# Kernel optimization log

Hardware: AMD Instinct MI355X
Metric: run time of the kernel (lower is better)

## Reference

```python
import jax, jax.numpy as jnp
import numpy as np

N = 20000      # nodes
E = 160000     # edges
F_IN = 64      # node_feature_dim
HID = 256      # hidden_dim (= per-head out_channels, concat=False)
HEADS = 4
OUT = 2
BN_EPS = 1e-5


def setup_inputs() -> dict:
    key = jax.random.key(0)
    ks = jax.random.split(key, 24)
    s = 0.02

    def w(k, shape):
        return jax.random.normal(k, shape, jnp.float32) * s

    return {
        "node_feature": jax.random.normal(ks[0], (N, F_IN), jnp.float32),
        "edge_index": jax.random.randint(ks[1], (2, E), 0, N, jnp.int32),
        # layer 1 (in=F_IN)
        "wq1": w(ks[2], (F_IN, HEADS * HID)), "bq1": w(ks[3], (HEADS * HID,)),
        "wk1": w(ks[4], (F_IN, HEADS * HID)), "bk1": w(ks[5], (HEADS * HID,)),
        "wv1": w(ks[6], (F_IN, HEADS * HID)), "bv1": w(ks[7], (HEADS * HID,)),
        "ws1": w(ks[8], (F_IN, HID)),        "bs1": w(ks[9], (HID,)),
        # layer 2 (in=HID)
        "wq2": w(ks[10], (HID, HEADS * HID)), "bq2": w(ks[11], (HEADS * HID,)),
        "wk2": w(ks[12], (HID, HEADS * HID)), "bk2": w(ks[13], (HEADS * HID,)),
        "wv2": w(ks[14], (HID, HEADS * HID)), "bv2": w(ks[15], (HEADS * HID,)),
        "ws2": w(ks[16], (HID, HID)),         "bs2": w(ks[17], (HID,)),
        # batch norm affine
        "bn_gamma": jnp.ones((HID,), jnp.float32) + w(ks[18], (HID,)),
        "bn_beta": w(ks[19], (HID,)),
        # final linear
        "lin_w": w(ks[20], (HID, OUT)), "lin_b": w(ks[21], (OUT,)),
    }


def _transformer_conv(x, src, dst, wq, bq, wk, bk, wv, bv, ws, bs):
    """PyG TransformerConv, heads=HEADS, concat=False (mean over heads), root_weight."""
    n = x.shape[0]
    q = (x @ wq + bq).reshape(n, HEADS, HID)   # [N,H,C]
    k = (x @ wk + bk).reshape(n, HEADS, HID)
    v = (x @ wv + bv).reshape(n, HEADS, HID)
    # per-edge attention logits: q_i . k_j / sqrt(C)   (message j->i, i = dst)
    alpha = jnp.einsum('ehc,ehc->eh', q[dst], k[src]) / jnp.sqrt(jnp.float32(HID))  # [E,H]
    # scatter-softmax over incoming edges of each target node
    m = jax.ops.segment_max(alpha, dst, num_segments=n)
    m = jnp.where(jnp.isfinite(m), m, 0.0)  # nodes with no in-edges
    ex = jnp.exp(alpha - m[dst])
    denom = jax.ops.segment_sum(ex, dst, num_segments=n)
    a = ex / (denom[dst] + 1e-16)                          # [E,H]
    out = jax.ops.segment_sum(v[src] * a[..., None], dst, num_segments=n)  # [N,H,C]
    return out.mean(axis=1) + x @ ws + bs                  # concat=False -> head mean; + skip


def reference(node_feature, edge_index,
              wq1, bq1, wk1, bk1, wv1, bv1, ws1, bs1,
              wq2, bq2, wk2, bk2, wv2, bv2, ws2, bs2,
              bn_gamma, bn_beta, lin_w, lin_b):
    src, dst = edge_index[0], edge_index[1]
    x = _transformer_conv(node_feature, src, dst, wq1, bq1, wk1, bk1, wv1, bv1, ws1, bs1)
    x = _transformer_conv(x, src, dst, wq2, bq2, wk2, bk2, wv2, bv2, ws2, bs2)
    # BatchNorm1d (training mode: batch statistics, biased variance)
    mu = x.mean(axis=0)
    var = jnp.mean(jnp.square(x - mu), axis=0)
    x = bn_gamma * (x - mu) / jnp.sqrt(var + BN_EPS) + bn_beta
    rsu_embedding = x[0:1]                     # [1, HID]
    logits = jax.nn.relu(x @ lin_w + lin_b)    # [N, OUT]
    action_prob = jax.nn.softmax(logits, axis=1)
    return (action_prob, rsu_embedding)
```

## Files before the change

### kernel.cpp

```cpp
#include <hip/hip_runtime.h>
#include <hip/hip_bf16.h>
#include <math.h>

#define DI __device__ __forceinline__

constexpr int NN   = 20000;
constexpr int NE   = 160000;
constexpr int FIN  = 64;
constexpr int HIDC = 256;

typedef __attribute__((ext_vector_type(8))) short short8;
typedef __attribute__((ext_vector_type(4))) float f32x4;

DI float bf2f(unsigned short u) { return __uint_as_float(((unsigned)u) << 16); }

DI void gld16(const void* g, void* l) {
  __builtin_amdgcn_global_load_lds((const __attribute__((address_space(1))) unsigned*)g,
                                   (__attribute__((address_space(3))) unsigned*)l, 16, 0, 0);
}

__global__ void k_prep(const float* __restrict__ x, __hip_bfloat16* __restrict__ xb,
                       const int* __restrict__ dst, int* __restrict__ deg) {
  int gid = blockIdx.x * 256 + threadIdx.x;
  if (gid < NN * FIN) xb[gid] = __float2bfloat16(x[gid]);
  if (gid < NE) atomicAdd(&deg[dst[gid]], 1);
}

__global__ void k_scan(const int* __restrict__ deg, int* __restrict__ offs,
                       int* __restrict__ cursor, int n_) {
  __shared__ int part[1024];
  int tid = threadIdx.x;
  const int CH = (n_ + 1023) >> 10;
  int base = tid * CH;
  int s = 0;
  for (int i = 0; i < CH; ++i) { int idx = base + i; if (idx < n_) s += deg[idx]; }
  part[tid] = s;
  __syncthreads();
  for (int off = 1; off < 1024; off <<= 1) {
    int v = (tid >= off) ? part[tid - off] : 0;
    __syncthreads();
    part[tid] += v;
    __syncthreads();
  }
  int run = (tid == 0) ? 0 : part[tid - 1];
  for (int i = 0; i < CH; ++i) {
    int idx = base + i;
    if (idx < n_) { offs[idx] = run; cursor[idx] = run; run += deg[idx]; }
  }
  if (tid == 1023) offs[n_] = run;
}

__global__ void k_scatter(const int* __restrict__ dst, int* __restrict__ cursor,
                          int* __restrict__ eid, int e_) {
  int e = blockIdx.x * blockDim.x + threadIdx.x;
  if (e < e_) {
    int p = atomicAdd(&cursor[dst[e]], 1);
    eid[p] = e;
  }
}

__global__ void k_sortsse(const int* __restrict__ offs, int* __restrict__ eid,
                          const int* __restrict__ src, int* __restrict__ sse, int n_) {
  int n = blockIdx.x * 256 + threadIdx.x;
  if (n >= n_) return;
  int s0 = offs[n], s1 = offs[n + 1];
  for (int i = s0 + 1; i < s1; ++i) {
    int v = eid[i];
    int j = i - 1;
    while (j >= s0 && eid[j] > v) { eid[j + 1] = eid[j]; --j; }
    eid[j + 1] = v;
  }
  for (int i = s0; i < s1; ++i) sse[i] = src[eid[i]];
}

__global__ void k_tr(const float* __restrict__ wq, const float* __restrict__ wk,
                     float* __restrict__ WqT, float* __restrict__ WkT, int IN_) {
  int gid = blockIdx.x * 256 + threadIdx.x;
  if (gid >= 1024 * IN_) return;
  int k = gid % IN_, j = gid / IN_;
  WqT[gid] = wq[(size_t)k * 1024 + j];
  WkT[gid] = wk[(size_t)k * 1024 + j];
}

template <int IN>
__global__ void k_mfill(const float* __restrict__ WqT, const float* __restrict__ WkT,
                        const float* __restrict__ bq, const float* __restrict__ bk,
                        const float* __restrict__ ws, const float* __restrict__ bs,
                        __hip_bfloat16* __restrict__ Wt, float* __restrict__ biasp) {
  constexpr int YW = 4 * IN;
  constexpr int CPB = 256 / IN;
  int k = threadIdx.x % IN;
  int sub = threadIdx.x / IN;
  int c = blockIdx.x * CPB + sub;
  float val = 0.f, bval = 0.f;
  if (c < YW) {
    int h = c / IN, i = c % IN;
    const float* wqp = WqT + (size_t)(h * 256) * IN + k;
    const float* wkp = WkT + (size_t)(h * 256) * IN + i;
    float s = 0.f;
#pragma unroll 4
    for (int j = 0; j < 256; ++j) s = fmaf(wqp[(size_t)j * IN], wkp[(size_t)j * IN], s);
    val = s;
  } else if (c < YW + 256) {
    int sc = c - YW;
    val = ws[(size_t)k * 256 + sc];
    bval = bs[sc];
  } else if (c < YW + 260) {
    int h = c - (YW + 256);
    const float* wqp = WqT + (size_t)(h * 256) * IN + k;
    const float* bkp = bk + h * 256;
    float s = 0.f;
#pragma unroll 4
    for (int j = 0; j < 256; ++j) s = fmaf(wqp[(size_t)j * IN], bkp[j], s);
    val = s;
    if (k == 0) {
      float bb = 0.f;
      for (int j = 0; j < 256; ++j) bb = fmaf(bq[h * 256 + j], bk[h * 256 + j], bb);
      bval = bb;
    }
  } else if (c < YW + 264) {
    int h = c - (YW + 260);
    const float* wkp = WkT + (size_t)(h * 256) * IN + k;
    const float* bqp = bq + h * 256;
    float s = 0.f;
#pragma unroll 4
    for (int j = 0; j < 256; ++j) s = fmaf(wkp[(size_t)j * IN], bqp[j], s);
    val = s;
  }
  Wt[(size_t)c * IN + k] = __float2bfloat16(val);
  if (k == 0) biasp[c] = bval;
}

template <int IN>
__global__ void k_pack2(const float* __restrict__ wv, const float* __restrict__ bv,
                        __hip_bfloat16* __restrict__ Wt2, float* __restrict__ bias2) {
  constexpr int K2 = 4 * IN;
  int gid = blockIdx.x * 256 + threadIdx.x;
  int col = gid / K2, k = gid % K2;
  int h = k / IN, d = k % IN;
  Wt2[gid] = __float2bfloat16(0.25f * wv[(size_t)d * 1024 + h * 256 + col]);
  if (k == 0)
    bias2[col] = 0.25f * (bv[col] + bv[256 + col] + bv[512 + col] + bv[768 + col]);
}

template <int IN>
__global__ __launch_bounds__(64, 2) void k_gemm1(
    const __hip_bfloat16* __restrict__ X, const __hip_bfloat16* __restrict__ Wt,
    const float* __restrict__ biasp,
    __hip_bfloat16* __restrict__ Ybuf, float* __restrict__ skipf,
    float* __restrict__ CDbuf, int nrows, int NCB, int NCH, int TPC, int RT) {
  __shared__ char lds[16384 + 2304];
  const int l = threadIdx.x;
  constexpr int K = IN;
  constexpr int YW = 4 * IN;
  const int nwg = NCB * NCH;
  const int per = nwg >> 3;
  const int w = (blockIdx.x & 7) * per + (blockIdx.x >> 3);
  const int chunk = w / NCB;
  const int ct = w % NCB;
  const int bn = ct * 64;
  const int t0 = chunk * TPC;
  int t1 = t0 + TPC; if (t1 > RT) t1 = RT;
  constexpr int KT = K / 64;
  constexpr int NS = K / 32;

  const int lm = l & 15, lk = l >> 4;

  short8 bfr[4 * NS];
  {
    const __hip_bfloat16* bp = Wt + (size_t)(bn + lm) * K + lk * 8;
#pragma unroll
    for (int n = 0; n < 4; ++n)
#pragma unroll
      for (int s = 0; s < NS; ++s)
        bfr[n * NS + s] = *(const short8*)(bp + (size_t)n * 16 * K + s * 32);
  }
  float bia[4];
#pragma unroll
  for (int n = 0; n < 4; ++n) bia[n] = biasp[bn + n * 16 + lm];

  const int mode = (bn < YW) ? 0 : ((bn < YW + 256) ? 1 : 2);

  const int jrow = l >> 3;
  const int cslot = (l & 7) ^ jrow;
  auto STAGE = [&](int buf, int t, int kt) {
    char* db = lds + buf * 8192;
#pragma unroll
    for (int j = 0; j < 8; ++j) {
      int r = t * 64 + j * 8 + jrow;
      if (r >= nrows) r = nrows - 1;
      gld16(X + (size_t)r * K + kt * 64 + cslot * 8, db + j * 1024 + l * 16);
    }
  };

  int buf = 0;
  STAGE(0, t0, 0);
  for (int t = t0; t < t1; ++t) {
    f32x4 acc[4][4] = {};
#pragma unroll
    for (int kt = 0; kt < KT; ++kt) {
      int nt = t, nk = kt + 1;
      if (nk == KT) { nt = (t + 1 < t1) ? t + 1 : t; nk = 0; }
      STAGE(buf ^ 1, nt, nk);
      asm volatile("s_waitcnt vmcnt(8)" ::: "memory");
      const char* db = lds + buf * 8192;
#pragma unroll
      for (int s2 = 0; s2 < 2; ++s2) {
        short8 a[4];
#pragma unroll
        for (int m = 0; m < 4; ++m) {
          int row = m * 16 + lm;
          a[m] = *(const short8*)(db + row * 128 + (((s2 * 4 + lk) ^ (lm & 7)) * 16));
        }
#pragma unroll
        for (int m = 0; m < 4; ++m)
#pragma unroll
          for (int n = 0; n < 4; ++n)
            acc[m][n] = __builtin_amdgcn_mfma_f32_16x16x32_bf16(
                a[m], bfr[n * NS + kt * 2 + s2], acc[m][n], 0, 0, 0);
      }
      buf ^= 1;
    }

    const int tbase = t * 64;
    if (mode == 0) {
      char* sc = lds + 16384;
      const int srow = l >> 2, qc = l & 3;
#pragma unroll
      for (int m = 0; m < 4; ++m) {
#pragma unroll
        for (int n = 0; n < 4; ++n)
#pragma unroll
          for (int r = 0; r < 4; ++r)
            *(__hip_bfloat16*)(sc + (lk * 4 + r) * 144 + (n * 16 + lm) * 2) =
                __float2bfloat16(acc[m][n][r] + bia[n]);
        const char* sr = sc + srow * 144 + qc * 32;
        short8 ta = *(const short8*)(sr);
        short8 tb = *(const short8*)(sr + 16);
        int grow = tbase + m * 16 + srow;
        if (grow < nrows) {
          ushort* o = (ushort*)Ybuf + (size_t)grow * YW + bn + qc * 16;
          *(short8*)o = ta;
          *(short8*)(o + 8) = tb;
        }
      }
    } else if (mode == 1) {
      const int cb = bn - YW;
#pragma unroll
      for (int m = 0; m < 4; ++m)
#pragma unroll
        for (int n = 0; n < 4; ++n)
#pragma unroll
          for (int r = 0; r < 4; ++r) {
            int row = tbase + m * 16 + lk * 4 + r;
            if (row < nrows) skipf[(size_t)row * HIDC + cb + n * 16 + lm] = acc[m][n][r] + bia[n];
          }
    } else {
#pragma unroll
      for (int m = 0; m < 4; ++m)
#pragma unroll
        for (int n = 0; n < 4; ++n) {
          int cl = n * 16 + lm;
          if (cl < 8) {
#pragma unroll
            for (int r = 0; r < 4; ++r) {
              int row = tbase + m * 16 + lk * 4 + r;
              if (row < nrows) CDbuf[(size_t)row * 8 + cl] = acc[m][n][r] + bia[n];
            }
          }
        }
    }
  }
  asm volatile("s_waitcnt vmcnt(0)" ::: "memory");
}

template <int IN, bool F32OUT>
__global__ __launch_bounds__(512) void k_attn_out(
    const __hip_bfloat16* __restrict__ Ybuf, const __hip_bfloat16* __restrict__ Xs,
    const float* __restrict__ CD, const int* __restrict__ offs,
    const int* __restrict__ sse, const __hip_bfloat16* __restrict__ Wt2,
    const float* __restrict__ bias2, const float* __restrict__ skipf,
    void* __restrict__ outp) {
  constexpr int K2 = 4 * IN;
  constexpr int DPL = IN / 16;
  constexpr int YW = 4 * IN;
  __shared__ __align__(16) char Zs[32 * K2 * 2];
  const int w = threadIdx.x >> 6, lane = threadIdx.x & 63;
  const int h4 = lane >> 4, j = lane & 15;
  const int nbase = blockIdx.x * 32;

  for (int u = 0; u < 4; ++u) {
    const int zrow = w * 4 + u;
    const int n = nbase + zrow;
    char* zp = Zs + zrow * (K2 * 2);
    const int sw = (zrow & 7) << 4;
    const int s0 = offs[n];
    const int deg = offs[n + 1] - s0;
    const int cb = (h4 * IN + j * DPL) * 2;

    if (deg == 0) {
      if constexpr (IN == 256) {
        short8 z8 = {};
        *(short8*)(zp + (cb ^ sw)) = z8;
        *(short8*)(zp + ((cb + 16) ^ sw)) = z8;
      } else {
        short4 z4 = {(short)0, (short)0, (short)0, (short)0};
        *(short4*)(zp + (cb ^ sw)) = z4;
      }
      continue;
    }

    float y[DPL];
    {
      const ushort* yr = (const ushort*)Ybuf + (size_t)n * YW + h4 * IN + j * DPL;
      if constexpr (IN == 256) {
        short8 y0 = *(const short8*)yr;
        short8 y1 = *(const short8*)(yr + 8);
#pragma unroll
        for (int d = 0; d < 8; ++d) {
          y[d] = bf2f((unsigned short)y0[d]);
          y[8 + d] = bf2f((unsigned short)y1[d]);
        }
      } else {
        short4 yv = *(const short4*)yr;
        y[0] = bf2f((unsigned short)yv.x);
        y[1] = bf2f((unsigned short)yv.y);
        y[2] = bf2f((unsigned short)yv.z);
        y[3] = bf2f((unsigned short)yv.w);
      }
    }
    float C = CD[(size_t)n * 8 + h4];
    float acc[DPL] = {};
    float denom = 0.f;
    const int* se = sse + s0;
    const ushort* xb = (const ushort*)Xs;

#define LOADE(P, E)                                                     \
  {                                                                     \
    int e_ = (E);                                                       \
    int s_ = se[(e_ < deg) ? e_ : 0];                                   \
    const ushort* xp_ = xb + (size_t)s_ * IN + j * DPL;                 \
    if constexpr (IN == 256) {                                          \
      P##0 = *(const short8*)xp_;                                       \
      P##1 = *(const short8*)(xp_ + 8);                                 \
    } else {                                                            \
      P##s = *(const short4*)xp_;                                       \
    }                                                                   \
    P##D = CD[(size_t)s_ * 8 + 4 + h4];                                 \
  }

#define COMPE(P, E)                                                     \
  {                                                                     \
    float xf[DPL];                                                      \
    if constexpr (IN == 256) {                                          \
      _Pragma("unroll") for (int d = 0; d < 8; ++d) {                   \
        xf[d] = bf2f((unsigned short)P##0[d]);                          \
        xf[8 + d] = bf2f((unsigned short)P##1[d]);                      \
      }                                                                 \
    } else {                                                            \
      xf[0] = bf2f((unsigned short)P##s.x);                             \
      xf[1] = bf2f((unsigned short)P##s.y);                             \
      xf[2] = bf2f((unsigned short)P##s.z);                             \
      xf[3] = bf2f((unsigned short)P##s.w);                             \
    }                                                                   \
    float p_ = 0.f;                                                     \
    _Pragma("unroll") for (int d = 0; d < DPL; ++d) p_ = fmaf(y[d], xf[d], p_); \
    p_ += __shfl_xor(p_, 1);                                            \
    p_ += __shfl_xor(p_, 2);                                            \
    p_ += __shfl_xor(p_, 4);                                            \
    p_ += __shfl_xor(p_, 8);                                            \
    float w_ = ((E) < deg) ? __expf((p_ + C + P##D) * 0.0625f) : 0.f;   \
    denom += w_;                                                        \
    _Pragma("unroll") for (int d = 0; d < DPL; ++d) acc[d] = fmaf(w_, xf[d], acc[d]); \
  }

    short8 A0, A1, B0, B1;
    short4 As, Bs;
    float AD, BD;
    (void)As; (void)Bs; (void)A0; (void)A1; (void)B0; (void)B1;
    LOADE(A, 0);
    for (int e = 0; e < deg; e += 2) {
      LOADE(B, e + 1);
      COMPE(A, e);
      LOADE(A, e + 2);
      COMPE(B, e + 1);
    }
#undef LOADE
#undef COMPE

    float dinv = 1.f / (denom + 1e-16f);
    if constexpr (IN == 256) {
      short8 o0, o1;
#pragma unroll
      for (int d = 0; d < 8; ++d) {
        o0[d] = (short)__bfloat16_as_ushort(__float2bfloat16(acc[d] * dinv));
        o1[d] = (short)__bfloat16_as_ushort(__float2bfloat16(acc[8 + d] * dinv));
      }
      *(short8*)(zp + (cb ^ sw)) = o0;
      *(short8*)(zp + ((cb + 16) ^ sw)) = o1;
    } else {
      short4 o;
      o.x = (short)__bfloat16_as_ushort(__float2bfloat16(acc[0] * dinv));
      o.y = (short)__bfloat16_as_ushort(__float2bfloat16(acc[1] * dinv));
      o.z = (short)__bfloat16_as_ushort(__float2bfloat16(acc[2] * dinv));
      o.w = (short)__bfloat16_as_ushort(__float2bfloat16(acc[3] * dinv));
      *(short4*)(zp + (cb ^ sw)) = o;
    }
  }
  __syncthreads();

  const int bn = w * 32;
  const int lm = lane & 15, lk = lane >> 4;
  constexpr int KT = K2 / 64;
  float bia[2];
#pragma unroll
  for (int n = 0; n < 2; ++n) bia[n] = bias2[bn + n * 16 + lm];
  const __hip_bfloat16* bp = Wt2 + (size_t)(bn + lm) * K2 + lk * 8;

  short8 bA[2][2], bB[2][2];
  f32x4 acc2[2][2] = {};

#define LOADB(D, CH)                                                        \
  {                                                                         \
    int ch_ = (CH);                                                         \
    _Pragma("unroll") for (int n = 0; n < 2; ++n)                           \
      _Pragma("unroll") for (int s2 = 0; s2 < 2; ++s2)                      \
        D[n][s2] = *(const short8*)(bp + (size_t)n * 16 * K2 + ch_ * 64 + s2 * 32); \
  }

#define COMPB(B, CH)                                                        \
  {                                                                         \
    int ch_ = (CH);                                                         \
    _Pragma("unroll") for (int s2 = 0; s2 < 2; ++s2) {                      \
      short8 a[2];                                                          \
      _Pragma("unroll") for (int m = 0; m < 2; ++m) {                       \
        int row = m * 16 + lm;                                              \
        a[m] = *(const short8*)(Zs + row * (K2 * 2) +                       \
                ((ch_ * 128 + s2 * 64 + lk * 16) ^ ((row & 7) << 4)));      \
      }                                                                     \
      _Pragma("unroll") for (int m = 0; m < 2; ++m)                         \
        _Pragma("unroll") for (int n = 0; n < 2; ++n)                       \
          acc2[m][n] = __builtin_amdgcn_mfma_f32_16x16x32_bf16(a[m], B[n][s2], acc2[m][n], 0, 0, 0); \
    }                                                                       \
  }

  LOADB(bA, 0);
  for (int ch = 0; ch < KT; ch += 2) {
    LOADB(bB, ch + 1);
    COMPB(bA, ch);
    if (ch + 2 < KT) LOADB(bA, ch + 2);
    COMPB(bB, ch + 1);
  }
#undef LOADB
#undef COMPB

#pragma unroll
  for (int m = 0; m < 2; ++m)
#pragma unroll
    for (int r = 0; r < 4; ++r) {
      int lr = m * 16 + lk * 4 + r;
      int g = nbase + lr;
      float af = (offs[g + 1] > offs[g]) ? 1.f : 0.f;
#pragma unroll
      for (int n = 0; n < 2; ++n) {
        int col = bn + n * 16 + lm;
        float v = acc2[m][n][r] + af * bia[n] + skipf[(size_t)g * HIDC + col];
        if constexpr (F32OUT)
          ((float*)outp)[(size_t)g * HIDC + col] = v;
        else
          ((ushort*)outp)[(size_t)g * HIDC + col] = __bfloat16_as_ushort(__float2bfloat16(v));
      }
    }
}

__global__ void k_bnstats(const float* __restrict__ x, float* __restrict__ psum,
                          float* __restrict__ psumsq) {
  int t = threadIdx.x, b = blockIdx.x;
  float s = 0.f, s2 = 0.f;
  for (int r = b; r < NN; r += 256) {
    float vv = x[(size_t)r * HIDC + t];
    s += vv; s2 += vv * vv;
  }
  psum[b * HIDC + t] = s;
  psumsq[b * HIDC + t] = s2;
}

__global__ void k_bnred(const float* __restrict__ psum, const float* __restrict__ psumsq,
                        float* __restrict__ sums, float* __restrict__ sumsq) {
  int t = threadIdx.x;
  float s = 0.f, s2 = 0.f;
  for (int b = 0; b < 256; ++b) { s += psum[b * HIDC + t]; s2 += psumsq[b * HIDC + t]; }
  sums[t] = s;
  sumsq[t] = s2;
}

__global__ __launch_bounds__(256) void k_final(
    const float* __restrict__ x, const float* __restrict__ sums, const float* __restrict__ sumsq,
    const float* __restrict__ gamma, const float* __restrict__ beta,
    const float* __restrict__ lw, const float* __restrict__ lb,
    float* __restrict__ out, int n_) {
  int sub = threadIdx.x >> 6, lane = threadIdx.x & 63;
  int n = blockIdx.x * 4 + sub;
  if (n >= n_) return;
  int c = lane * 4;
  float4 sm  = *(const float4*)(sums + c);
  float4 sq  = *(const float4*)(sumsq + c);
  const float inv_n = 1.f / (float)n_;
  float mu0 = sm.x * inv_n, mu1 = sm.y * inv_n, mu2 = sm.z * inv_n, mu3 = sm.w * inv_n;
  float r0 = 1.f / sqrtf(fmaxf(sq.x * inv_n - mu0 * mu0, 0.f) + 1e-5f);
  float r1 = 1.f / sqrtf(fmaxf(sq.y * inv_n - mu1 * mu1, 0.f) + 1e-5f);
  float r2 = 1.f / sqrtf(fmaxf(sq.z * inv_n - mu2 * mu2, 0.f) + 1e-5f);
  float r3 = 1.f / sqrtf(fmaxf(sq.w * inv_n - mu3 * mu3, 0.f) + 1e-5f);
  const float* xr = x + (size_t)n * HIDC;
  float4 xv = *(const float4*)(xr + c);
  float4 gv = *(const float4*)(gamma + c);
  float4 bv = *(const float4*)(beta + c);
  float y0 = gv.x * (xv.x - mu0) * r0 + bv.x;
  float y1 = gv.y * (xv.y - mu1) * r1 + bv.y;
  float y2 = gv.z * (xv.z - mu2) * r2 + bv.z;
  float y3 = gv.w * (xv.w - mu3) * r3 + bv.w;
  float4 wa = *(const float4*)(lw + (size_t)c * 2);
  float4 wb = *(const float4*)(lw + (size_t)c * 2 + 4);
  float p0 = y0 * wa.x + y1 * wa.z + y2 * wb.x + y3 * wb.z;
  float p1 = y0 * wa.y + y1 * wa.w + y2 * wb.y + y3 * wb.w;
#pragma unroll
  for (int off = 32; off > 0; off >>= 1) {
    p0 += __shfl_xor(p0, off);
    p1 += __shfl_xor(p1, off);
  }
  if (n == 0) *(float4*)(out + (size_t)NN * 2 + c) = make_float4(y0, y1, y2, y3);
  if (lane == 0) {
    float l0 = fmaxf(p0 + lb[0], 0.f);
    float l1 = fmaxf(p1 + lb[1], 0.f);
    float m = fmaxf(l0, l1);
    float e0 = expf(l0 - m), e1 = expf(l1 - m);
    float inv = 1.f / (e0 + e1);
    out[(size_t)n * 2 + 0] = e0 * inv;
    out[(size_t)n * 2 + 1] = e1 * inv;
  }
}

extern "C" void kernel_launch(void* const* d_in, const int* in_sizes, int n_in,
                              void* d_out, int out_size, void* d_ws, size_t ws_size,
                              hipStream_t stream) {
  const float* x0  = (const float*)d_in[0];
  const int*   ei  = (const int*)d_in[1];
  const float* wq1 = (const float*)d_in[2];  const float* bq1 = (const float*)d_in[3];
  const float* wk1 = (const float*)d_in[4];  const float* bk1 = (const float*)d_in[5];
  const float* wv1 = (const float*)d_in[6];  const float* bv1 = (const float*)d_in[7];
  const float* ws1 = (const float*)d_in[8];  const float* bs1 = (const float*)d_in[9];
  const float* wq2 = (const float*)d_in[10]; const float* bq2 = (const float*)d_in[11];
  const float* wk2 = (const float*)d_in[12]; const float* bk2 = (const float*)d_in[13];
  const float* wv2 = (const float*)d_in[14]; const float* bv2 = (const float*)d_in[15];
  const float* ws2 = (const float*)d_in[16]; const float* bs2 = (const float*)d_in[17];
  const float* gam = (const float*)d_in[18]; const float* bet = (const float*)d_in[19];
  const float* lw  = (const float*)d_in[20]; const float* lb  = (const float*)d_in[21];
  const int* srcv = ei;
  const int* dstv = ei + NE;

  char* p = (char*)d_ws;
  auto take = [&](size_t bytes) {
    char* r = p;
    p += (bytes + 255) & ~(size_t)255;
    return r;
  };
  __hip_bfloat16* Ybuf = (__hip_bfloat16*)take((size_t)NN * 1024 * 2);
  float* skipf = (float*)take((size_t)NN * HIDC * 4);
  float* x3    = (float*)take((size_t)NN * HIDC * 4);
  __hip_bfloat16* x0b = (__hip_bfloat16*)take((size_t)NN * FIN * 2);
  __hip_bfloat16* x2b = (__hip_bfloat16*)take((size_t)NN * HIDC * 2);
  float* CDbuf = (float*)take((size_t)NN * 8 * 4);
  __hip_bfloat16* Wt1a = (__hip_bfloat16*)take((size_t)576 * 64 * 2);
  __hip_bfloat16* Wt1b = (__hip_bfloat16*)take((size_t)1344 * 256 * 2);
  float* bias1a = (float*)take(576 * 4);
  float* bias1b = (float*)take(1344 * 4);
  __hip_bfloat16* Wt2a = (__hip_bfloat16*)take((size_t)256 * 256 * 2);
  __hip_bfloat16* Wt2b = (__hip_bfloat16*)take((size_t)256 * 1024 * 2);
  float* bias2a = (float*)take(256 * 4);
  float* bias2b = (float*)take(256 * 4);
  float* WqTa = (float*)take((size_t)1024 * 64 * 4);
  float* WkTa = (float*)take((size_t)1024 * 64 * 4);
  float* WqTb = (float*)take((size_t)1024 * 256 * 4);
  float* WkTb = (float*)take((size_t)1024 * 256 * 4);
  float* psum  = (float*)take(256 * HIDC * 4);
  float* psumsq= (float*)take(256 * HIDC * 4);
  float* bnbuf = (float*)take(2 * HIDC * 4);
  int* deg    = (int*)take((size_t)NN * 4);
  int* offs   = (int*)take((size_t)(NN + 1) * 4);
  int* cursor = (int*)take((size_t)NN * 4);
  int* eidb   = (int*)take((size_t)NE * 4);
  int* sse    = (int*)take((size_t)NE * 4);
  if ((size_t)(p - (char*)d_ws) > ws_size) return;

  float* sums  = bnbuf;
  float* sumsq = bnbuf + HIDC;

  hipMemsetAsync(deg, 0, (size_t)NN * 4, stream);
  k_prep<<<(NN * FIN + 255) / 256, 256, 0, stream>>>(x0, x0b, dstv, deg);
  k_scan<<<1, 1024, 0, stream>>>(deg, offs, cursor, NN);
  k_scatter<<<(NE + 255) / 256, 256, 0, stream>>>(dstv, cursor, eidb, NE);
  k_sortsse<<<(NN + 255) / 256, 256, 0, stream>>>(offs, eidb, srcv, sse, NN);

  k_tr<<<(1024 * 64 + 255) / 256, 256, 0, stream>>>(wq1, wk1, WqTa, WkTa, 64);
  k_mfill<64><<<144, 256, 0, stream>>>(WqTa, WkTa, bq1, bk1, ws1, bs1, Wt1a, bias1a);
  k_pack2<64><<<256, 256, 0, stream>>>(wv1, bv1, Wt2a, bias2a);
  k_tr<<<(1024 * 256 + 255) / 256, 256, 0, stream>>>(wq2, wk2, WqTb, WkTb, 256);
  k_mfill<256><<<1344, 256, 0, stream>>>(WqTb, WkTb, bq2, bk2, ws2, bs2, Wt1b, bias1b);
  k_pack2<256><<<1024, 256, 0, stream>>>(wv2, bv2, Wt2b, bias2b);

  const int RT  = (NN + 63) / 64;
  const int NCH = 40;
  const int TPC = (RT + NCH - 1) / NCH;
  const int AG = NN / 32;

  k_gemm1<64><<<9 * NCH, 64, 0, stream>>>(x0b, Wt1a, bias1a, Ybuf, skipf, CDbuf, NN, 9, NCH, TPC, RT);
  k_attn_out<64, false><<<AG, 512, 0, stream>>>(Ybuf, x0b, CDbuf, offs, sse, Wt2a, bias2a, skipf, x2b);
  k_gemm1<256><<<21 * NCH, 64, 0, stream>>>(x2b, Wt1b, bias1b, Ybuf, skipf, CDbuf, NN, 21, NCH, TPC, RT);
  k_attn_out<256, true><<<AG, 512, 0, stream>>>(Ybuf, x2b, CDbuf, offs, sse, Wt2b, bias2b, skipf, x3);
  k_bnstats<<<256, 256, 0, stream>>>(x3, psum, psumsq);
  k_bnred<<<1, 256, 0, stream>>>(psum, psumsq, sums, sumsq);
  k_final<<<(NN + 3) / 4, 256, 0, stream>>>(x3, sums, sumsq, gam, bet, lw, lb, (float*)d_out, NN);
}
```

Baseline: 389.3 us.

## Shrink attention-GEMM tile to 16 nodes with 4 waves covering 64 columns each

The fused attention+output GEMM kernel now processes 16 nodes per block with 256 threads instead of 32 nodes with 512 threads. Each wave computes 64 output columns for one 16-row MFMA tile, so each A fragment from LDS feeds four MFMAs. The LDS layout of the aggregated Z rows is remapped so the K index matches the MFMA operand order. This halves LDS per block and doubles the grid for better occupancy, but each block reloads the full weight matrix for fewer rows, doubling weight traffic per node.

```diff
diff --git a/kernel.cpp b/kernel.cpp
--- a/kernel.cpp
+++ b/kernel.cpp
@@ -275,7 +275,7 @@
 }
 
 template <int IN, bool F32OUT>
-__global__ __launch_bounds__(512) void k_attn_out(
+__global__ __launch_bounds__(256, 4) void k_attn_gemm(
     const __hip_bfloat16* __restrict__ Ybuf, const __hip_bfloat16* __restrict__ Xs,
     const float* __restrict__ CD, const int* __restrict__ offs,
     const int* __restrict__ sse, const __hip_bfloat16* __restrict__ Wt2,
@@ -284,28 +284,29 @@
   constexpr int K2 = 4 * IN;
   constexpr int DPL = IN / 16;
   constexpr int YW = 4 * IN;
-  __shared__ __align__(16) char Zs[32 * K2 * 2];
+  constexpr int RS = K2 * 2;
+  __shared__ __align__(16) char Zs[16 * RS];
   const int w = threadIdx.x >> 6, lane = threadIdx.x & 63;
   const int h4 = lane >> 4, j = lane & 15;
-  const int nbase = blockIdx.x * 32;
+  const int nbase = blockIdx.x * 16;
 
   for (int u = 0; u < 4; ++u) {
     const int zrow = w * 4 + u;
     const int n = nbase + zrow;
-    char* zp = Zs + zrow * (K2 * 2);
+    char* zp = Zs + zrow * RS;
     const int sw = (zrow & 7) << 4;
     const int s0 = offs[n];
     const int deg = offs[n + 1] - s0;
-    const int cb = (h4 * IN + j * DPL) * 2;
+    const int lslot = (h4 * 16 + j);
 
     if (deg == 0) {
       if constexpr (IN == 256) {
         short8 z8 = {};
-        *(short8*)(zp + (cb ^ sw)) = z8;
-        *(short8*)(zp + ((cb + 16) ^ sw)) = z8;
+        *(short8*)(zp + ((lslot * 16) ^ sw)) = z8;
+        *(short8*)(zp + ((1024 + lslot * 16) ^ sw)) = z8;
       } else {
         short4 z4 = {(short)0, (short)0, (short)0, (short)0};
-        *(short4*)(zp + (cb ^ sw)) = z4;
+        *(short4*)(zp + ((lslot * 8) ^ sw)) = z4;
       }
       continue;
     }
@@ -396,34 +397,34 @@
         o0[d] = (short)__bfloat16_as_ushort(__float2bfloat16(acc[d] * dinv));
         o1[d] = (short)__bfloat16_as_ushort(__float2bfloat16(acc[8 + d] * dinv));
       }
-      *(short8*)(zp + (cb ^ sw)) = o0;
-      *(short8*)(zp + ((cb + 16) ^ sw)) = o1;
+      *(short8*)(zp + ((lslot * 16) ^ sw)) = o0;
+      *(short8*)(zp + ((1024 + lslot * 16) ^ sw)) = o1;
     } else {
       short4 o;
       o.x = (short)__bfloat16_as_ushort(__float2bfloat16(acc[0] * dinv));
       o.y = (short)__bfloat16_as_ushort(__float2bfloat16(acc[1] * dinv));
       o.z = (short)__bfloat16_as_ushort(__float2bfloat16(acc[2] * dinv));
       o.w = (short)__bfloat16_as_ushort(__float2bfloat16(acc[3] * dinv));
-      *(short4*)(zp + (cb ^ sw)) = o;
+      *(short4*)(zp + ((lslot * 8) ^ sw)) = o;
     }
   }
   __syncthreads();
 
-  const int bn = w * 32;
+  const int bn = w * 64;
   const int lm = lane & 15, lk = lane >> 4;
   constexpr int KT = K2 / 64;
-  float bia[2];
-#pragma unroll
-  for (int n = 0; n < 2; ++n) bia[n] = bias2[bn + n * 16 + lm];
+  float bia[4];
+#pragma unroll
+  for (int n = 0; n < 4; ++n) bia[n] = bias2[bn + n * 16 + lm];
   const __hip_bfloat16* bp = Wt2 + (size_t)(bn + lm) * K2 + lk * 8;
 
-  short8 bA[2][2], bB[2][2];
-  f32x4 acc2[2][2] = {};
+  short8 bA[4][2], bB[4][2];
+  f32x4 acc2[4] = {};
 
 #define LOADB(D, CH)                                                        \
   {                                                                         \
     int ch_ = (CH);                                                         \
-    _Pragma("unroll") for (int n = 0; n < 2; ++n)                           \
+    _Pragma("unroll") for (int n = 0; n < 4; ++n)                           \
       _Pragma("unroll") for (int s2 = 0; s2 < 2; ++s2)                      \
         D[n][s2] = *(const short8*)(bp + (size_t)n * 16 * K2 + ch_ * 64 + s2 * 32); \
   }
@@ -432,15 +433,16 @@
   {                                                                         \
     int ch_ = (CH);                                                         \
     _Pragma("unroll") for (int s2 = 0; s2 < 2; ++s2) {                      \
-      short8 a[2];                                                          \
-      _Pragma("unroll") for (int m = 0; m < 2; ++m) {                       \
-        int row = m * 16 + lm;                                              \
-        a[m] = *(const short8*)(Zs + row * (K2 * 2) +                       \
-                ((ch_ * 128 + s2 * 64 + lk * 16) ^ ((row & 7) << 4)));      \
-      }                                                                     \
-      _Pragma("unroll") for (int m = 0; m < 2; ++m)                         \
-        _Pragma("unroll") for (int n = 0; n < 2; ++n)                       \
-          acc2[m][n] = __builtin_amdgcn_mfma_f32_16x16x32_bf16(a[m], B[n][s2], acc2[m][n], 0, 0, 0); \
+      int c0 = ch_ * 64 + s2 * 32 + lk * 8;                                 \
+      int zoff;                                                             \
+      if constexpr (IN == 256)                                              \
+        zoff = ((c0 & 8) << 7) + ((c0 >> 8) << 8) + (((c0 >> 4) & 15) << 4); \
+      else                                                                  \
+        zoff = c0 * 2;                                                      \
+      int row = lm;                                                         \
+      short8 a = *(const short8*)(Zs + row * RS + (zoff ^ ((row & 7) << 4))); \
+      _Pragma("unroll") for (int n = 0; n < 4; ++n)                         \
+        acc2[n] = __builtin_amdgcn_mfma_f32_16x16x32_bf16(a, B[n][s2], acc2[n], 0, 0, 0); \
     }                                                                       \
   }
 
@@ -455,22 +457,20 @@
 #undef COMPB
 
 #pragma unroll
-  for (int m = 0; m < 2; ++m)
-#pragma unroll
-    for (int r = 0; r < 4; ++r) {
-      int lr = m * 16 + lk * 4 + r;
-      int g = nbase + lr;
-      float af = (offs[g + 1] > offs[g]) ? 1.f : 0.f;
-#pragma unroll
-      for (int n = 0; n < 2; ++n) {
-        int col = bn + n * 16 + lm;
-        float v = acc2[m][n][r] + af * bia[n] + skipf[(size_t)g * HIDC + col];
-        if constexpr (F32OUT)
-          ((float*)outp)[(size_t)g * HIDC + col] = v;
-        else
-          ((ushort*)outp)[(size_t)g * HIDC + col] = __bfloat16_as_ushort(__float2bfloat16(v));
-      }
-    }
+  for (int r = 0; r < 4; ++r) {
+    int lr = lk * 4 + r;
+    int g = nbase + lr;
+    float af = (offs[g + 1] > offs[g]) ? 1.f : 0.f;
+#pragma unroll
+    for (int n = 0; n < 4; ++n) {
+      int col = bn + n * 16 + lm;
+      float v = acc2[n][r] + af * bia[n] + skipf[(size_t)g * HIDC + col];
+      if constexpr (F32OUT)
+        ((float*)outp)[(size_t)g * HIDC + col] = v;
+      else
+        ((ushort*)outp)[(size_t)g * HIDC + col] = __bfloat16_as_ushort(__float2bfloat16(v));
+    }
+  }
 }
 
 __global__ void k_bnstats(const float* __restrict__ x, float* __restrict__ psum,
@@ -611,12 +611,12 @@
   const int RT  = (NN + 63) / 64;
   const int NCH = 40;
   const int TPC = (RT + NCH - 1) / NCH;
-  const int AG = NN / 32;
+  const int AG = NN / 16;
 
   k_gemm1<64><<<9 * NCH, 64, 0, stream>>>(x0b, Wt1a, bias1a, Ybuf, skipf, CDbuf, NN, 9, NCH, TPC, RT);
-  k_attn_out<64, false><<<AG, 512, 0, stream>>>(Ybuf, x0b, CDbuf, offs, sse, Wt2a, bias2a, skipf, x2b);
+  k_attn_gemm<64, false><<<AG, 256, 0, stream>>>(Ybuf, x0b, CDbuf, offs, sse, Wt2a, bias2a, skipf, x2b);
   k_gemm1<256><<<21 * NCH, 64, 0, stream>>>(x2b, Wt1b, bias1b, Ybuf, skipf, CDbuf, NN, 21, NCH, TPC, RT);
-  k_attn_out<256, true><<<AG, 512, 0, stream>>>(Ybuf, x2b, CDbuf, offs, sse, Wt2b, bias2b, skipf, x3);
+  k_attn_gemm<256, true><<<AG, 256, 0, stream>>>(Ybuf, x2b, CDbuf, offs, sse, Wt2b, bias2b, skipf, x3);
   k_bnstats<<<256, 256, 0, stream>>>(x3, psum, psumsq);
   k_bnred<<<1, 256, 0, stream>>>(psum, psumsq, sums, sumsq);
   k_final<<<(NN + 3) / 4, 256, 0, stream>>>(x3, sums, sumsq, gam, bet, lw, lb, (float*)d_out, NN);
```

New measurement: 427.0 us. +9.7%, slower.
